# Kernel optimization log

Hardware: AMD Instinct MI355X
Metric: run time of the kernel (lower is better)

The kernel has to match this reference:

```python
import jax, jax.numpy as jnp
import numpy as np
import math

D = 1024
FFN = 4096
NHEADS = 8
HEAD_DIM = D // NHEADS
RL_DIM = 4
LN_EPS = 1e-5


def _layer_norm(x, gamma, beta):
    mu = jnp.mean(x, axis=-1, keepdims=True)
    var = jnp.var(x, axis=-1, keepdims=True)
    return (x - mu) * jax.lax.rsqrt(var + LN_EPS) * gamma + beta


def setup_inputs() -> dict:
    key = jax.random.key(0)
    ks = jax.random.split(key, 12)
    B, L = 2, 2048
    s = 1.0 / math.sqrt(D)
    inp = {
        "h": jax.random.normal(ks[0], (B, L, D), dtype=jnp.float32),
        "rh": jax.random.normal(ks[1], (B, L, RL_DIM), dtype=jnp.float32),
        "Wq": jax.random.normal(ks[2], (D, D), dtype=jnp.float32) * s,
        "Wk": jax.random.normal(ks[3], (D, D), dtype=jnp.float32) * s,
        "Wv": jax.random.normal(ks[4], (D, D), dtype=jnp.float32) * s,
        "Wo": jax.random.normal(ks[5], (D, D), dtype=jnp.float32) * s,
        "Wrk": jax.random.normal(ks[6], (RL_DIM, RL_DIM), dtype=jnp.float32) * 0.5,
        "Wrq": jax.random.normal(ks[7], (RL_DIM, RL_DIM), dtype=jnp.float32) * 0.5,
        "W1": jax.random.normal(ks[8], (D, FFN), dtype=jnp.float32) * s,
        "b1": jnp.zeros((FFN,), dtype=jnp.float32),
        "W2": jax.random.normal(ks[9], (FFN, D), dtype=jnp.float32) / math.sqrt(FFN),
        "b2": jnp.zeros((D,), dtype=jnp.float32),
        "g1": jnp.ones((D,), dtype=jnp.float32),
        "be1": jnp.zeros((D,), dtype=jnp.float32),
        "g2": jnp.ones((D,), dtype=jnp.float32),
        "be2": jnp.zeros((D,), dtype=jnp.float32),
    }
    return inp


def reference(h, rh, Wq, Wk, Wv, Wo, Wrk, Wrq, W1, b1, W2, b2, g1, be1, g2, be2):
    B, L, _ = h.shape
    q = h @ Wq  # [B, L, D]
    k = h @ Wk
    v = h @ Wv
    # Faithful to the torch code: .view() reshapes (NOT transposes).
    q_ = q.reshape(B, NHEADS, L, HEAD_DIM)
    k_ = k.reshape(B, NHEADS, L, HEAD_DIM)
    v_ = v.reshape(B, NHEADS, L, HEAD_DIM)
    k_t = k_.reshape(B, NHEADS, HEAD_DIM, L)  # reshape, not transpose, as in source
    score = jnp.einsum("bnld,bndm->bnlm", q_, k_t) / math.sqrt(HEAD_DIM)
    # relative-position bias (rl=True path)
    r_k = rh @ Wrk  # [B, L, rl_dim]
    r_q = rh @ Wrq
    r_q_ = r_q[:, None]  # [B, 1, L, rl_dim]
    r_k_t = r_k[:, None].reshape(B, 1, RL_DIM, L)  # reshape, as in source
    score = score + jnp.einsum("bnlr,bnrm->bnlm", r_q_, r_k_t) / 2.0
    attn = jax.nn.softmax(score, axis=-1)
    context = jnp.einsum("bnlm,bnmd->bnld", attn, v_)
    h_sa = context.reshape(B, L, D) @ Wo
    h1 = _layer_norm(h_sa + h, g1, be1)
    hf = jax.nn.relu(h1 @ W1 + b1) @ W2 + b2
    h2 = _layer_norm(h1 + hf, g2, be2)
    return h2
```

## Files before the change

### kernel.cpp

```cpp
#include <hip/hip_runtime.h>

typedef __bf16 bf16;
typedef __bf16 bf16x8 __attribute__((ext_vector_type(8)));
typedef __bf16 bf16x4 __attribute__((ext_vector_type(4)));
typedef float  f32x4  __attribute__((ext_vector_type(4)));

#define D_     1024
#define FFN_   4096
#define NH_    8
#define HD_    128
#define L_     2048
#define B_     2
#define ROWS_  4096
#define PAIRS_ 16
#define KT_    64
#define PSTR   72
#define ALPHA_  0.08838834764831845f
#define RSCALE_ 5.656854249492381f

__device__ __forceinline__ void async16(const bf16* g, bf16* l) {
    __builtin_amdgcn_global_load_lds(
        (const __attribute__((address_space(1))) unsigned int*)g,
        (__attribute__((address_space(3))) unsigned int*)l, 16, 0, 0);
}
__device__ __forceinline__ f32x4 MFMA(bf16x8 a, bf16x8 b, f32x4 c) {
    return __builtin_amdgcn_mfma_f32_16x16x32_bf16(a, b, c, 0, 0, 0);
}

__global__ void cvt_bf16_kernel(const float* __restrict__ in, bf16* __restrict__ out) {
    long i = ((long)blockIdx.x * 256 + threadIdx.x) * 4;
    float4 v = *(const float4*)(in + i);
    bf16x4 o = {(bf16)v.x, (bf16)v.y, (bf16)v.z, (bf16)v.w};
    *(bf16x4*)(out + i) = o;
}

template<typename TI>
__global__ void transpose_to_bf16(const TI* __restrict__ in, bf16* __restrict__ out,
                                  int r, int c, long sIn, long sOut) {
    __shared__ bf16 t[32][33];
    long zi = (long)blockIdx.z * sIn;
    long zo = (long)blockIdx.z * sOut;
    int x0 = blockIdx.x * 32, y0 = blockIdx.y * 32;
    int tx = threadIdx.x & 31, ty = threadIdx.x >> 5;
#pragma unroll
    for (int i = 0; i < 4; i++)
        t[ty + i * 8][tx] = (bf16)in[zi + (long)(y0 + ty + i * 8) * c + x0 + tx];
    __syncthreads();
#pragma unroll
    for (int i = 0; i < 4; i++)
        out[zo + (long)(x0 + ty + i * 8) * r + y0 + tx] = t[tx][ty + i * 8];
}

__global__ void rqk_kernel(const float* __restrict__ rh, const float* __restrict__ Wrq,
                           const float* __restrict__ Wrk, float* __restrict__ rq,
                           float* __restrict__ rk) {
    int t = blockIdx.x * 256 + threadIdx.x;
    float4 r = *(const float4*)(rh + (long)t * 4);
    float q[4], k[4];
#pragma unroll
    for (int c = 0; c < 4; c++) {
        q[c] = r.x * Wrq[c] + r.y * Wrq[4 + c] + r.z * Wrq[8 + c] + r.w * Wrq[12 + c];
        k[c] = r.x * Wrk[c] + r.y * Wrk[4 + c] + r.z * Wrk[8 + c] + r.w * Wrk[12 + c];
    }
    float4 qo = {q[0], q[1], q[2], q[3]};
    float4 ko = {k[0], k[1], k[2], k[3]};
    *(float4*)(rq + (long)t * 4) = qo;
    *(float4*)(rk + (long)t * 4) = ko;
}

template<int BM, int EPI>
__launch_bounds__(256)
__global__ void gemm128(const bf16* __restrict__ A, const bf16* __restrict__ Bt,
                        void* __restrict__ Cv, const float* __restrict__ bias,
                        int M, int N, int K, int lda, int ldb,
                        long sA, long sB, long sC, float alpha) {
    constexpr int RF = (BM == 128) ? 4 : 2;
    __shared__ __align__(16) bf16 As[BM * 32];
    __shared__ __align__(16) bf16 Bs[128 * 32];
    const int tid  = threadIdx.x;
    const int wave = tid >> 6, lane = tid & 63;
    const int quad = lane >> 4, mr = lane & 15;
    const int bM = blockIdx.x * BM, bN = blockIdx.y * 128;
    A  += (long)blockIdx.z * sA;
    Bt += (long)blockIdx.z * sB;
    const int wr = (wave >> 1) * (BM / 2), wc = (wave & 1) * 64;

    f32x4 acc[RF][4];
#pragma unroll
    for (int r = 0; r < RF; r++)
#pragma unroll
        for (int c = 0; c < 4; c++) { f32x4 z = {0.f, 0.f, 0.f, 0.f}; acc[r][c] = z; }

    const int scol = (lane & 3) * 8;
    const bf16* Ag0; const bf16* Ag1 = nullptr;
    if (BM == 128) {
        const int srow = wave * 32 + (lane >> 2);
        Ag0 = A + (long)(bM + srow) * lda + scol;
        Ag1 = Ag0 + (long)16 * lda;
    } else {
        const int srow = wave * 16 + (lane >> 2);
        Ag0 = A + (long)(bM + srow) * lda + scol;
    }
    const int srowB = wave * 32 + (lane >> 2);
    const bf16* Bg0 = Bt + (long)(bN + srowB) * ldb + scol;
    const bf16* Bg1 = Bg0 + (long)16 * ldb;
    bf16* AsW = As + wave * (BM == 128 ? 1024 : 512);
    bf16* BsW = Bs + wave * 1024;

    for (int k0 = 0; k0 < K; k0 += 32) {
        if (BM == 128) { async16(Ag0, AsW); async16(Ag1, AsW + 512); Ag0 += 32; Ag1 += 32; }
        else           { async16(Ag0, AsW); Ag0 += 32; }
        async16(Bg0, BsW); async16(Bg1, BsW + 512);
        Bg0 += 32; Bg1 += 32;
        __syncthreads();
        bf16x8 af[RF], bfv[4];
#pragma unroll
        for (int r = 0; r < RF; r++)
            af[r] = *(const bf16x8*)(&As[(wr + r * 16 + mr) * 32 + quad * 8]);
#pragma unroll
        for (int c = 0; c < 4; c++)
            bfv[c] = *(const bf16x8*)(&Bs[(wc + c * 16 + mr) * 32 + quad * 8]);
#pragma unroll
        for (int r = 0; r < RF; r++)
#pragma unroll
            for (int c = 0; c < 4; c++)
                acc[r][c] = MFMA(af[r], bfv[c], acc[r][c]);
        __syncthreads();
    }

    const long zC = (long)blockIdx.z * sC;
    float bias_c[4];
    if (EPI & 1) {
#pragma unroll
        for (int c = 0; c < 4; c++) bias_c[c] = bias[bN + wc + c * 16 + mr];
    }
#pragma unroll
    for (int r = 0; r < RF; r++) {
#pragma unroll
        for (int c = 0; c < 4; c++) {
            const long col = bN + wc + c * 16 + mr;
#pragma unroll
            for (int i = 0; i < 4; i++) {
                const long row = bM + wr + r * 16 + quad * 4 + i;
                float v = acc[r][c][i] * alpha;
                if (EPI & 1) v += bias_c[c];
                if (EPI & 2) v = fmaxf(v, 0.f);
                if (EPI & 4) ((bf16*)Cv)[zC + row * (long)N + col] = (bf16)v;
                else         ((float*)Cv)[zC + row * (long)N + col] = v;
            }
        }
    }
}

template<int EPI>
__launch_bounds__(512, 2)
__global__ void gemm256(const bf16* __restrict__ A, const bf16* __restrict__ Bt,
                        void* __restrict__ Cv, const float* __restrict__ bias,
                        int M, int N, int K, int lda, int ldb,
                        long sA, long sB, long sC, float alpha) {
    __shared__ __align__(16) bf16 LA[4][256 * 32];
    __shared__ __align__(16) bf16 LB[4][256 * 32];
    const int tid = threadIdx.x, wave = tid >> 6, lane = tid & 63;
    const int quad = lane >> 4, mr = lane & 15;
    const int wr = wave >> 2, wc = wave & 3;
    const int bM = blockIdx.x * 256, bN = blockIdx.y * 256;
    (void)M;
    A  += (long)blockIdx.z * sA;
    Bt += (long)blockIdx.z * sB;

    const int srow = tid >> 2;
    const int sg   = (((tid & 3) ^ ((tid >> 3) & 3))) * 8;
    const bf16* Ag = A  + (long)(bM + srow) * lda + sg;
    const bf16* Bg = Bt + (long)(bN + srow) * ldb + sg;

    auto stageA = [&](int slot, int kt) {
        const bf16* s = Ag + kt * 32;
        async16(s,                   &LA[slot][wave * 512]);
        async16(s + (long)128 * lda, &LA[slot][4096 + wave * 512]);
    };
    auto stageB = [&](int slot, int kt) {
        const bf16* s = Bg + kt * 32;
        async16(s,                   &LB[slot][wave * 512]);
        async16(s + (long)128 * ldb, &LB[slot][4096 + wave * 512]);
    };

    f32x4 acc[8][4];
#pragma unroll
    for (int f = 0; f < 8; f++)
#pragma unroll
        for (int n = 0; n < 4; n++) { f32x4 z = {0.f, 0.f, 0.f, 0.f}; acc[f][n] = z; }

    const int gsw = (quad ^ ((mr >> 1) & 3)) * 8;

    stageA(0, 0); stageB(0, 0);
    stageA(1, 1); stageB(1, 1);
    stageA(2, 2); stageB(2, 2);
    asm volatile("s_waitcnt vmcnt(8)" ::: "memory");
    __builtin_amdgcn_s_barrier();

    const int NT = K >> 5;
    for (int t = 0; t < NT; ++t) {
        const int slot = t & 3;
        const bf16* As = &LA[slot][0];
        const bf16* Bs = &LB[slot][0];

        bf16x8 a0[4], bb[4];
#pragma unroll
        for (int f = 0; f < 4; f++)
            a0[f] = *(const bf16x8*)(As + (wr * 128 + f * 16 + mr) * 32 + gsw);
#pragma unroll
        for (int n = 0; n < 4; n++)
            bb[n] = *(const bf16x8*)(Bs + (wc * 64 + n * 16 + mr) * 32 + gsw);
        if (t + 3 < NT) stageA((t + 3) & 3, t + 3);
        __builtin_amdgcn_s_barrier();
        asm volatile("s_waitcnt lgkmcnt(0)" ::: "memory");
        __builtin_amdgcn_sched_barrier(0);
        __builtin_amdgcn_s_setprio(1);
#pragma unroll
        for (int f = 0; f < 4; f++)
#pragma unroll
            for (int n = 0; n < 4; n++)
                acc[f][n] = MFMA(a0[f], bb[n], acc[f][n]);
        __builtin_amdgcn_s_setprio(0);
        __builtin_amdgcn_s_barrier();

        bf16x8 a1[4];
#pragma unroll
        for (int f = 0; f < 4; f++)
            a1[f] = *(const bf16x8*)(As + (wr * 128 + 64 + f * 16 + mr) * 32 + gsw);
        if (t + 3 < NT) stageB((t + 3) & 3, t + 3);
        __builtin_amdgcn_s_barrier();
        asm volatile("s_waitcnt lgkmcnt(0)" ::: "memory");
        __builtin_amdgcn_sched_barrier(0);
        __builtin_amdgcn_s_setprio(1);
#pragma unroll
        for (int f = 0; f < 4; f++)
#pragma unroll
            for (int n = 0; n < 4; n++)
                acc[4 + f][n] = MFMA(a1[f], bb[n], acc[4 + f][n]);
        __builtin_amdgcn_s_setprio(0);
        if (t < NT - 3)       asm volatile("s_waitcnt vmcnt(8)" ::: "memory");
        else if (t == NT - 3) asm volatile("s_waitcnt vmcnt(4)" ::: "memory");
        else if (t == NT - 2) asm volatile("s_waitcnt vmcnt(0)" ::: "memory");
        __builtin_amdgcn_s_barrier();
    }

    const long zC = (long)blockIdx.z * sC;
    float bias_c[4];
    if (EPI & 1) {
#pragma unroll
        for (int n = 0; n < 4; n++) bias_c[n] = bias[bN + wc * 64 + n * 16 + mr];
    }
#pragma unroll
    for (int f = 0; f < 8; f++) {
#pragma unroll
        for (int n = 0; n < 4; n++) {
            const long col = bN + wc * 64 + n * 16 + mr;
#pragma unroll
            for (int i = 0; i < 4; i++) {
                const long row = bM + wr * 128 + f * 16 + quad * 4 + i;
                float v = acc[f][n][i] * alpha;
                if (EPI & 1) v += bias_c[n];
                if (EPI & 2) v = fmaxf(v, 0.f);
                if (EPI & 4) ((bf16*)Cv)[zC + row * (long)N + col] = (bf16)v;
                else         ((float*)Cv)[zC + row * (long)N + col] = v;
            }
        }
    }
}

template<int SPLIT>
__launch_bounds__(256, 1)
__global__ void flash_attn(const bf16* __restrict__ qb, const bf16* __restrict__ kT,
                           const bf16* __restrict__ vT, const float* __restrict__ rq,
                           const float* __restrict__ rk, bf16* __restrict__ ctx,
                           float* __restrict__ opart, float* __restrict__ osum) {
    __shared__ __align__(16) bf16  Ksh[KT_ * HD_];
    __shared__ __align__(16) bf16  Vsh[HD_ * KT_];
    __shared__ __align__(16) float rks[4 * KT_];
    __shared__ __align__(16) bf16  Ps[4][32 * PSTR];

    const int tid = threadIdx.x, wave = tid >> 6, lane = tid & 63;
    const int quad = lane >> 4, mr = lane & 15;
    const int nwg = 256 * SPLIT;
    const int lid = blockIdx.x + (blockIdx.y << 4) + (blockIdx.z << 8);
    const int wid = (lid & 7) * (nwg >> 3) + (lid >> 3);
    const int ksp = wid >> 8;
    const int pair = (wid >> 4) & 15, b = pair >> 3;
    const int bQ = (wid & 15) * 128;
    const long PB = (long)pair * L_ * HD_;
    const bf16* Qg = qb + PB;
    const bf16* Kg = kT + PB;
    const bf16* Vg = vT + PB;
    const float* rkb = rk + (long)b * L_ * 4;

    bf16x8 Qf[2][4], Qe[2];
#pragma unroll
    for (int f = 0; f < 2; f++) {
#pragma unroll
        for (int t = 0; t < 4; t++)
            Qf[f][t] = *(const bf16x8*)(Qg + (long)(bQ + wave * 32 + f * 16 + mr) * HD_ + t * 32 + quad * 8);
        bf16x8 z = {};
        if (quad == 0) {
            float4 v = *(const float4*)(rq + ((long)b * L_ + bQ + wave * 32 + f * 16 + mr) * 4);
            z[0] = (bf16)(v.x * RSCALE_); z[1] = (bf16)(v.y * RSCALE_);
            z[2] = (bf16)(v.z * RSCALE_); z[3] = (bf16)(v.w * RSCALE_);
        }
        Qe[f] = z;
    }

    bf16x8 ones;
#pragma unroll
    for (int j = 0; j < 8; j++) ones[j] = (bf16)1.0f;

    f32x4 O[2][8], Os[2];
#pragma unroll
    for (int f = 0; f < 2; f++) {
#pragma unroll
        for (int c = 0; c < 8; c++) { f32x4 z = {0.f, 0.f, 0.f, 0.f}; O[f][c] = z; }
        f32x4 z = {0.f, 0.f, 0.f, 0.f}; Os[f] = z;
    }

    const int tile0 = ksp * ((L_ / KT_) / SPLIT);
    const int tile1 = tile0 + (L_ / KT_) / SPLIT;
    for (int kt = tile0; kt < tile1; kt++) {
        const int kt0 = kt * KT_;
#pragma unroll
        for (int it = 0; it < 4; it++) {
            int G = it * 256 + tid;
            int r1 = G >> 4, g1 = (G & 15) ^ (r1 & 15);
            async16(Kg + (long)(kt0 + r1) * HD_ + g1 * 8, &Ksh[(it * 256 + wave * 64) * 8]);
            int r2 = G >> 3, g2 = (G & 7) ^ (r2 & 7);
            async16(Vg + (long)r2 * L_ + kt0 + g2 * 8, &Vsh[(it * 256 + wave * 64) * 8]);
        }
        if (tid < 64) {
            int r3 = tid >> 4, g3 = tid & 15;
            async16((const bf16*)(rkb + (long)r3 * L_ + kt0 + g3 * 4), (bf16*)&rks[0]);
        }
        __syncthreads();

        bf16* PsW = Ps[wave];

        f32x4 sc[4][2];
        __builtin_amdgcn_s_setprio(1);
#pragma unroll
        for (int c = 0; c < 4; c++) {
            f32x4 s0 = {0.f, 0.f, 0.f, 0.f}, s1 = s0;
#pragma unroll
            for (int t = 0; t < 4; t++) {
                bf16x8 kf = *(const bf16x8*)(Ksh + (c * 16 + mr) * HD_ + (((t * 4 + quad) ^ mr) * 8));
                s0 = MFMA(Qf[0][t], kf, s0);
                s1 = MFMA(Qf[1][t], kf, s1);
            }
            bf16x8 ke = {};
            if (quad == 0) {
                ke[0] = (bf16)rks[0 * KT_ + c * 16 + mr];
                ke[1] = (bf16)rks[1 * KT_ + c * 16 + mr];
                ke[2] = (bf16)rks[2 * KT_ + c * 16 + mr];
                ke[3] = (bf16)rks[3 * KT_ + c * 16 + mr];
            }
            s0 = MFMA(Qe[0], ke, s0);
            s1 = MFMA(Qe[1], ke, s1);
            sc[c][0] = s0; sc[c][1] = s1;
        }
        __builtin_amdgcn_s_setprio(0);

#pragma unroll
        for (int f = 0; f < 2; f++) {
#pragma unroll
            for (int i = 0; i < 4; i++) {
                const int prow = (f * 16 + quad * 4 + i) * PSTR;
                PsW[prow + 0 * 16 + mr] = (bf16)__expf(sc[0][f][i] * ALPHA_);
                PsW[prow + 1 * 16 + mr] = (bf16)__expf(sc[1][f][i] * ALPHA_);
                PsW[prow + 2 * 16 + mr] = (bf16)__expf(sc[2][f][i] * ALPHA_);
                PsW[prow + 3 * 16 + mr] = (bf16)__expf(sc[3][f][i] * ALPHA_);
            }
        }

        __builtin_amdgcn_s_setprio(1);
#pragma unroll
        for (int t = 0; t < 2; t++) {
            bf16x8 pf0 = *(const bf16x8*)(PsW + (0 * 16 + mr) * PSTR + t * 32 + quad * 8);
            bf16x8 pf1 = *(const bf16x8*)(PsW + (1 * 16 + mr) * PSTR + t * 32 + quad * 8);
            Os[0] = MFMA(pf0, ones, Os[0]);
            Os[1] = MFMA(pf1, ones, Os[1]);
#pragma unroll
            for (int c2 = 0; c2 < 8; c2++) {
                bf16x8 vf = *(const bf16x8*)(Vsh + (c2 * 16 + mr) * KT_ + (((t * 4 + quad) ^ (mr & 7)) * 8));
                O[0][c2] = MFMA(pf0, vf, O[0][c2]);
                O[1][c2] = MFMA(pf1, vf, O[1][c2]);
            }
        }
        __builtin_amdgcn_s_setprio(0);
        __syncthreads();
    }

    if (SPLIT == 1) {
        bf16* Cg = ctx + PB;
#pragma unroll
        for (int f = 0; f < 2; f++)
#pragma unroll
            for (int i = 0; i < 4; i++) {
                const float inv = 1.f / Os[f][i];
                const long row = bQ + wave * 32 + f * 16 + quad * 4 + i;
#pragma unroll
                for (int c2 = 0; c2 < 8; c2++)
                    Cg[row * HD_ + c2 * 16 + mr] = (bf16)(O[f][c2][i] * inv);
            }
    } else {
        float* Og = opart + (long)ksp * ((long)PAIRS_ * L_ * HD_) + PB;
        float* Sg = osum + (long)ksp * (PAIRS_ * L_) + pair * L_;
#pragma unroll
        for (int f = 0; f < 2; f++)
#pragma unroll
            for (int i = 0; i < 4; i++) {
                const long row = bQ + wave * 32 + f * 16 + quad * 4 + i;
#pragma unroll
                for (int c2 = 0; c2 < 8; c2++)
                    Og[row * HD_ + c2 * 16 + mr] = O[f][c2][i];
                if (mr == 0) Sg[row] = Os[f][i];
            }
    }
}

template<int KS>
__global__ void flash_reduce(const float* __restrict__ op, const float* __restrict__ os,
                             bf16* __restrict__ ctx) {
    const long PLHD = (long)PAIRS_ * L_ * HD_;
    long e = ((long)blockIdx.x * 256 + threadIdx.x) * 4;
    long row = e >> 7;
    float4 a = *(const float4*)(op + e);
    float s = os[row];
#pragma unroll
    for (int z = 1; z < KS; z++) {
        float4 p = *(const float4*)(op + (long)z * PLHD + e);
        a.x += p.x; a.y += p.y; a.z += p.z; a.w += p.w;
        s += os[(long)z * PAIRS_ * L_ + row];
    }
    float inv = 1.f / s;
    bf16x4 o = {(bf16)(a.x * inv), (bf16)(a.y * inv),
                (bf16)(a.z * inv), (bf16)(a.w * inv)};
    *(bf16x4*)(ctx + e) = o;
}

__global__ void layernorm_res(const float* __restrict__ x1, const float* __restrict__ x2,
                              const float* __restrict__ g, const float* __restrict__ be,
                              float* __restrict__ outf, bf16* __restrict__ outb) {
    const int row = blockIdx.x, tid = threadIdx.x;
    const long base = (long)row * D_ + tid * 4;
    float4 a = *(const float4*)(x1 + base);
    float4 b = *(const float4*)(x2 + base);
    float x[4] = {a.x + b.x, a.y + b.y, a.z + b.z, a.w + b.w};
    float s = x[0] + x[1] + x[2] + x[3];
    float s2 = x[0] * x[0] + x[1] * x[1] + x[2] * x[2] + x[3] * x[3];
#pragma unroll
    for (int off = 32; off; off >>= 1) { s += __shfl_xor(s, off, 64); s2 += __shfl_xor(s2, off, 64); }
    __shared__ float ps[4], ps2[4];
    int wave = tid >> 6, lane = tid & 63;
    if (lane == 0) { ps[wave] = s; ps2[wave] = s2; }
    __syncthreads();
    s  = ps[0] + ps[1] + ps[2] + ps[3];
    s2 = ps2[0] + ps2[1] + ps2[2] + ps2[3];
    float mean = s * (1.f / D_);
    float var  = s2 * (1.f / D_) - mean * mean;
    float rstd = rsqrtf(var + 1e-5f);
    float4 gg = *(const float4*)(g + tid * 4);
    float4 bb = *(const float4*)(be + tid * 4);
    float y0 = (x[0] - mean) * rstd * gg.x + bb.x;
    float y1 = (x[1] - mean) * rstd * gg.y + bb.y;
    float y2 = (x[2] - mean) * rstd * gg.z + bb.z;
    float y3 = (x[3] - mean) * rstd * gg.w + bb.w;
    float4 yo = {y0, y1, y2, y3};
    *(float4*)(outf + base) = yo;
    bf16x4 ob = {(bf16)y0, (bf16)y1, (bf16)y2, (bf16)y3};
    *(bf16x4*)(outb + base) = ob;
}

template<int SK>
__global__ void layernorm_res2(const float* __restrict__ parts, const float* __restrict__ b2,
                               const float* __restrict__ x2, const float* __restrict__ g,
                               const float* __restrict__ be, float* __restrict__ outf) {
    const int row = blockIdx.x, tid = threadIdx.x;
    const long base = (long)row * D_ + tid * 4;
    float4 a = *(const float4*)(parts + base);
#pragma unroll
    for (int z = 1; z < SK; z++) {
        float4 p = *(const float4*)(parts + (long)z * ROWS_ * D_ + base);
        a.x += p.x; a.y += p.y; a.z += p.z; a.w += p.w;
    }
    float4 bb2 = *(const float4*)(b2 + tid * 4);
    float4 b = *(const float4*)(x2 + base);
    float x[4] = {a.x + bb2.x + b.x, a.y + bb2.y + b.y, a.z + bb2.z + b.z, a.w + bb2.w + b.w};
    float s = x[0] + x[1] + x[2] + x[3];
    float s2 = x[0] * x[0] + x[1] * x[1] + x[2] * x[2] + x[3] * x[3];
#pragma unroll
    for (int off = 32; off; off >>= 1) { s += __shfl_xor(s, off, 64); s2 += __shfl_xor(s2, off, 64); }
    __shared__ float ps[4], ps2[4];
    int wave = tid >> 6, lane = tid & 63;
    if (lane == 0) { ps[wave] = s; ps2[wave] = s2; }
    __syncthreads();
    s  = ps[0] + ps[1] + ps[2] + ps[3];
    s2 = ps2[0] + ps2[1] + ps2[2] + ps2[3];
    float mean = s * (1.f / D_);
    float var  = s2 * (1.f / D_) - mean * mean;
    float rstd = rsqrtf(var + 1e-5f);
    float4 gg = *(const float4*)(g + tid * 4);
    float4 bb = *(const float4*)(be + tid * 4);
    float4 yo = {(x[0] - mean) * rstd * gg.x + bb.x, (x[1] - mean) * rstd * gg.y + bb.y,
                 (x[2] - mean) * rstd * gg.z + bb.z, (x[3] - mean) * rstd * gg.w + bb.w};
    *(float4*)(outf + base) = yo;
}

extern "C" void kernel_launch(void* const* d_in, const int* in_sizes, int n_in,
                              void* d_out, int out_size, void* d_ws, size_t ws_size,
                              hipStream_t stream) {
    (void)in_sizes; (void)n_in; (void)out_size;
    const float* h   = (const float*)d_in[0];
    const float* rh  = (const float*)d_in[1];
    const float* Wq  = (const float*)d_in[2];
    const float* Wk  = (const float*)d_in[3];
    const float* Wv  = (const float*)d_in[4];
    const float* Wo  = (const float*)d_in[5];
    const float* Wrk = (const float*)d_in[6];
    const float* Wrq = (const float*)d_in[7];
    const float* W1  = (const float*)d_in[8];
    const float* b1  = (const float*)d_in[9];
    const float* W2  = (const float*)d_in[10];
    const float* b2  = (const float*)d_in[11];
    const float* g1  = (const float*)d_in[12];
    const float* be1 = (const float*)d_in[13];
    const float* g2  = (const float*)d_in[14];
    const float* be2 = (const float*)d_in[15];

    char* w = (char*)d_ws;
    size_t used = 0;
    auto alloc = [&](size_t bytes) { char* p = w + used; used += (bytes + 255) & ~(size_t)255; return p; };
    bf16*  hb   = (bf16*)alloc((size_t)ROWS_ * D_ * 2);
    bf16*  Wqt  = (bf16*)alloc((size_t)D_ * D_ * 2);
    bf16*  Wkt  = (bf16*)alloc((size_t)D_ * D_ * 2);
    bf16*  Wvt  = (bf16*)alloc((size_t)D_ * D_ * 2);
    bf16*  Wot  = (bf16*)alloc((size_t)D_ * D_ * 2);
    bf16*  W1t  = (bf16*)alloc((size_t)D_ * FFN_ * 2);
    bf16*  W2t  = (bf16*)alloc((size_t)FFN_ * D_ * 2);
    bf16*  qb   = (bf16*)alloc((size_t)ROWS_ * D_ * 2);
    bf16*  kb   = (bf16*)alloc((size_t)ROWS_ * D_ * 2);
    bf16*  vb   = (bf16*)alloc((size_t)ROWS_ * D_ * 2);
    bf16*  kT   = (bf16*)alloc((size_t)ROWS_ * D_ * 2);
    bf16*  vT   = (bf16*)alloc((size_t)ROWS_ * D_ * 2);
    float* rq   = (float*)alloc((size_t)ROWS_ * 4 * 4);
    float* rk   = (float*)alloc((size_t)ROWS_ * 4 * 4);
    float* h1   = (float*)alloc((size_t)ROWS_ * D_ * 4);

    const size_t psz    = (size_t)ROWS_ * D_ * 4;
    const size_t PLHD   = (size_t)PAIRS_ * L_ * HD_;
    const size_t needKS = 2 * PLHD * 4 + 2 * (size_t)PAIRS_ * L_ * 4;
    const size_t avail  = (ws_size > used) ? ws_size - used : 0;
    const int SK = (avail >= 4 * psz) ? 4 : (avail >= 2 * psz) ? 2 : 1;
    size_t region = (size_t)SK * psz;
    const int KS = (avail >= (needKS > region ? needKS : region)) ? 2 : 1;
    if (KS == 2 && needKS > region) region = needKS;
    float* P = (float*)alloc(region);
    float* hsa   = P;
    float* Opart = P;
    float* Osum  = P + 2 * PLHD;
    bf16* ctx = hb;
    bf16* mid = qb;
    bf16* h1b = hb;

    const dim3 blk(256);
    const dim3 blk512(512);
    const long BH = (long)L_ * HD_;

    cvt_bf16_kernel<<<ROWS_ * D_ / 1024, blk, 0, stream>>>(h, hb);
    transpose_to_bf16<float><<<dim3(32, 32, 1), blk, 0, stream>>>(Wq, Wqt, D_, D_, 0, 0);
    transpose_to_bf16<float><<<dim3(32, 32, 1), blk, 0, stream>>>(Wk, Wkt, D_, D_, 0, 0);
    transpose_to_bf16<float><<<dim3(32, 32, 1), blk, 0, stream>>>(Wv, Wvt, D_, D_, 0, 0);
    transpose_to_bf16<float><<<dim3(32, 32, 1), blk, 0, stream>>>(Wo, Wot, D_, D_, 0, 0);
    transpose_to_bf16<float><<<dim3(128, 32, 1), blk, 0, stream>>>(W1, W1t, D_, FFN_, 0, 0);
    transpose_to_bf16<float><<<dim3(32, 128, 1), blk, 0, stream>>>(W2, W2t, FFN_, D_, 0, 0);
    rqk_kernel<<<ROWS_ / 256, blk, 0, stream>>>(rh, Wrq, Wrk, rq, rk);
    gemm256<4><<<dim3(16, 4, 3), blk512, 0, stream>>>(hb, Wqt, qb, nullptr,
        ROWS_, D_, D_, D_, D_, 0, (long)D_ * D_, (long)ROWS_ * D_, 1.f);
    transpose_to_bf16<bf16><<<dim3(64, 4, PAIRS_), blk, 0, stream>>>(kb, kT, HD_, L_, BH, BH);
    transpose_to_bf16<bf16><<<dim3(4, 64, PAIRS_), blk, 0, stream>>>(vb, vT, L_, HD_, BH, BH);
    if (KS == 2) {
        flash_attn<2><<<dim3(16, 16, 2), blk, 0, stream>>>(qb, kT, vT, rq, rk, ctx, Opart, Osum);
        flash_reduce<2><<<PAIRS_ * L_ * HD_ / 1024, blk, 0, stream>>>(Opart, Osum, ctx);
    } else {
        flash_attn<1><<<dim3(16, 16, 1), blk, 0, stream>>>(qb, kT, vT, rq, rk, ctx, Opart, Osum);
    }
    gemm128<64, 0><<<dim3(64, 8, 1), blk, 0, stream>>>(ctx, Wot, hsa, nullptr,
        ROWS_, D_, D_, D_, D_, 0, 0, 0, 1.f);
    layernorm_res<<<ROWS_, blk, 0, stream>>>(hsa, h, g1, be1, h1, h1b);
    gemm256<7><<<dim3(16, 16, 1), blk512, 0, stream>>>(h1b, W1t, mid, b1,
        ROWS_, FFN_, D_, D_, D_, 0, 0, 0, 1.f);
    {
        const int KC = FFN_ / SK;
        if (SK == 4) {
            gemm256<0><<<dim3(16, 4, 4), blk512, 0, stream>>>(mid, W2t, P, nullptr,
                ROWS_, D_, KC, FFN_, FFN_, KC, KC, (long)ROWS_ * D_, 1.f);
            layernorm_res2<4><<<ROWS_, blk, 0, stream>>>(P, b2, h1, g2, be2, (float*)d_out);
        } else if (SK == 2) {
            gemm256<0><<<dim3(16, 4, 2), blk512, 0, stream>>>(mid, W2t, P, nullptr,
                ROWS_, D_, KC, FFN_, FFN_, KC, KC, (long)ROWS_ * D_, 1.f);
            layernorm_res2<2><<<ROWS_, blk, 0, stream>>>(P, b2, h1, g2, be2, (float*)d_out);
        } else {
            gemm128<128, 0><<<dim3(32, 8, 1), blk, 0, stream>>>(mid, W2t, P, nullptr,
                ROWS_, D_, FFN_, FFN_, FFN_, 0, 0, 0, 1.f);
            layernorm_res2<1><<<ROWS_, blk, 0, stream>>>(P, b2, h1, g2, be2, (float*)d_out);
        }
    }
}
```

Measured before the change: 382.6 us.

## Double-buffer flash attention K/V tiles with smaller key tile, retile Wo GEMM

The flash attention kernel now uses a 32-key tile with two LDS buffers, so the async load of the next K, V and rk tile is issued before computing on the current one, and a single waitcnt plus barrier replaces the per-tile syncthreads. The aim is to hide global-to-LDS load latency behind MFMA and exp work. The cost is twice as many loop iterations with less MFMA work per barrier. Separately, the output-projection GEMM switches from the 64-row to the 128-row gemm128 tiling with half the blocks.

```diff
diff --git a/kernel.cpp b/kernel.cpp
--- a/kernel.cpp
+++ b/kernel.cpp
@@ -13,8 +13,8 @@
 #define B_     2
 #define ROWS_  4096
 #define PAIRS_ 16
-#define KT_    64
-#define PSTR   72
+#define KT_    32
+#define PSTR   40
 #define ALPHA_  0.08838834764831845f
 #define RSCALE_ 5.656854249492381f
 
@@ -275,9 +275,9 @@
                            const bf16* __restrict__ vT, const float* __restrict__ rq,
                            const float* __restrict__ rk, bf16* __restrict__ ctx,
                            float* __restrict__ opart, float* __restrict__ osum) {
-    __shared__ __align__(16) bf16  Ksh[KT_ * HD_];
-    __shared__ __align__(16) bf16  Vsh[HD_ * KT_];
-    __shared__ __align__(16) float rks[4 * KT_];
+    __shared__ __align__(16) bf16  Ksh[2][KT_ * HD_];
+    __shared__ __align__(16) bf16  Vsh[2][HD_ * KT_];
+    __shared__ __align__(16) float rks[2][4 * KT_];
     __shared__ __align__(16) bf16  Ps[4][32 * PSTR];
 
     const int tid = threadIdx.x, wave = tid >> 6, lane = tid & 63;
@@ -294,6 +294,21 @@
     const bf16* Vg = vT + PB;
     const float* rkb = rk + (long)b * L_ * 4;
 
+    auto stage = [&](int bn, int kn0) {
+#pragma unroll
+        for (int it = 0; it < 2; it++) {
+            int G = it * 256 + tid;
+            int r1 = G >> 4, g1 = (G & 15) ^ (r1 & 15);
+            async16(Kg + (long)(kn0 + r1) * HD_ + g1 * 8, &Ksh[bn][(it * 256 + wave * 64) * 8]);
+            int r2 = G >> 2, g2 = (G & 3) ^ (r2 & 3);
+            async16(Vg + (long)r2 * L_ + kn0 + g2 * 8, &Vsh[bn][(it * 256 + wave * 64) * 8]);
+        }
+        if (tid < 32) {
+            int r3 = tid >> 3, g3 = tid & 7;
+            async16((const bf16*)(rkb + (long)r3 * L_ + kn0 + g3 * 4), (bf16*)&rks[bn][0]);
+        }
+    };
+
     bf16x8 Qf[2][4], Qe[2];
 #pragma unroll
     for (int f = 0; f < 2; f++) {
@@ -323,41 +338,38 @@
 
     const int tile0 = ksp * ((L_ / KT_) / SPLIT);
     const int tile1 = tile0 + (L_ / KT_) / SPLIT;
+
+    stage(tile0 & 1, tile0 * KT_);
+    asm volatile("s_waitcnt vmcnt(0)" ::: "memory");
+    __builtin_amdgcn_s_barrier();
+
     for (int kt = tile0; kt < tile1; kt++) {
-        const int kt0 = kt * KT_;
-#pragma unroll
-        for (int it = 0; it < 4; it++) {
-            int G = it * 256 + tid;
-            int r1 = G >> 4, g1 = (G & 15) ^ (r1 & 15);
-            async16(Kg + (long)(kt0 + r1) * HD_ + g1 * 8, &Ksh[(it * 256 + wave * 64) * 8]);
-            int r2 = G >> 3, g2 = (G & 7) ^ (r2 & 7);
-            async16(Vg + (long)r2 * L_ + kt0 + g2 * 8, &Vsh[(it * 256 + wave * 64) * 8]);
-        }
-        if (tid < 64) {
-            int r3 = tid >> 4, g3 = tid & 15;
-            async16((const bf16*)(rkb + (long)r3 * L_ + kt0 + g3 * 4), (bf16*)&rks[0]);
-        }
-        __syncthreads();
+        const int cur = kt & 1;
+        const bool hn = (kt + 1 < tile1);
+        if (hn) stage(cur ^ 1, (kt + 1) * KT_);
 
         bf16* PsW = Ps[wave];
-
-        f32x4 sc[4][2];
+        const bf16*  Kcur = Ksh[cur];
+        const bf16*  Vcur = Vsh[cur];
+        const float* rkc  = rks[cur];
+
+        f32x4 sc[2][2];
         __builtin_amdgcn_s_setprio(1);
 #pragma unroll
-        for (int c = 0; c < 4; c++) {
+        for (int c = 0; c < 2; c++) {
             f32x4 s0 = {0.f, 0.f, 0.f, 0.f}, s1 = s0;
 #pragma unroll
             for (int t = 0; t < 4; t++) {
-                bf16x8 kf = *(const bf16x8*)(Ksh + (c * 16 + mr) * HD_ + (((t * 4 + quad) ^ mr) * 8));
+                bf16x8 kf = *(const bf16x8*)(Kcur + (c * 16 + mr) * HD_ + (((t * 4 + quad) ^ mr) * 8));
                 s0 = MFMA(Qf[0][t], kf, s0);
                 s1 = MFMA(Qf[1][t], kf, s1);
             }
             bf16x8 ke = {};
             if (quad == 0) {
-                ke[0] = (bf16)rks[0 * KT_ + c * 16 + mr];
-                ke[1] = (bf16)rks[1 * KT_ + c * 16 + mr];
-                ke[2] = (bf16)rks[2 * KT_ + c * 16 + mr];
-                ke[3] = (bf16)rks[3 * KT_ + c * 16 + mr];
+                ke[0] = (bf16)rkc[0 * KT_ + c * 16 + mr];
+                ke[1] = (bf16)rkc[1 * KT_ + c * 16 + mr];
+                ke[2] = (bf16)rkc[2 * KT_ + c * 16 + mr];
+                ke[3] = (bf16)rkc[3 * KT_ + c * 16 + mr];
             }
             s0 = MFMA(Qe[0], ke, s0);
             s1 = MFMA(Qe[1], ke, s1);
@@ -372,27 +384,28 @@
                 const int prow = (f * 16 + quad * 4 + i) * PSTR;
                 PsW[prow + 0 * 16 + mr] = (bf16)__expf(sc[0][f][i] * ALPHA_);
                 PsW[prow + 1 * 16 + mr] = (bf16)__expf(sc[1][f][i] * ALPHA_);
-                PsW[prow + 2 * 16 + mr] = (bf16)__expf(sc[2][f][i] * ALPHA_);
-                PsW[prow + 3 * 16 + mr] = (bf16)__expf(sc[3][f][i] * ALPHA_);
             }
         }
 
         __builtin_amdgcn_s_setprio(1);
-#pragma unroll
-        for (int t = 0; t < 2; t++) {
-            bf16x8 pf0 = *(const bf16x8*)(PsW + (0 * 16 + mr) * PSTR + t * 32 + quad * 8);
-            bf16x8 pf1 = *(const bf16x8*)(PsW + (1 * 16 + mr) * PSTR + t * 32 + quad * 8);
+        {
+            bf16x8 pf0 = *(const bf16x8*)(PsW + (0 * 16 + mr) * PSTR + quad * 8);
+            bf16x8 pf1 = *(const bf16x8*)(PsW + (1 * 16 + mr) * PSTR + quad * 8);
             Os[0] = MFMA(pf0, ones, Os[0]);
             Os[1] = MFMA(pf1, ones, Os[1]);
 #pragma unroll
             for (int c2 = 0; c2 < 8; c2++) {
-                bf16x8 vf = *(const bf16x8*)(Vsh + (c2 * 16 + mr) * KT_ + (((t * 4 + quad) ^ (mr & 7)) * 8));
+                bf16x8 vf = *(const bf16x8*)(Vcur + (c2 * 16 + mr) * KT_ + ((quad ^ (mr & 3)) * 8));
                 O[0][c2] = MFMA(pf0, vf, O[0][c2]);
                 O[1][c2] = MFMA(pf1, vf, O[1][c2]);
             }
         }
         __builtin_amdgcn_s_setprio(0);
-        __syncthreads();
+
+        if (hn) {
+            asm volatile("s_waitcnt vmcnt(0)" ::: "memory");
+            __builtin_amdgcn_s_barrier();
+        }
     }
 
     if (SPLIT == 1) {
@@ -589,7 +602,7 @@
     } else {
         flash_attn<1><<<dim3(16, 16, 1), blk, 0, stream>>>(qb, kT, vT, rq, rk, ctx, Opart, Osum);
     }
-    gemm128<64, 0><<<dim3(64, 8, 1), blk, 0, stream>>>(ctx, Wot, hsa, nullptr,
+    gemm128<128, 0><<<dim3(32, 8, 1), blk, 0, stream>>>(ctx, Wot, hsa, nullptr,
         ROWS_, D_, D_, D_, D_, 0, 0, 0, 1.f);
     layernorm_res<<<ROWS_, blk, 0, stream>>>(hsa, h, g1, be1, h1, h1b);
     gemm256<7><<<dim3(16, 16, 1), blk512, 0, stream>>>(h1b, W1t, mid, b1,
```

New measurement: 395.0 us. +3.2%, slower.

## Replace 256x256 GEMM with 128x256 tile, 4-wave, double-buffered kernel

Applied to the files above, without the earlier changes.

Swaps the 512-thread 256x256 GEMM, which used a 4-stage async LDS pipeline and split A halves, for a 256-thread kernel computing 128x256 tiles. Each wave owns a 64-column slice across all 128 rows, and the kernel uses simple two-slot double buffering with one barrier per k-step. Grids double in the x dimension, and the Wo projection GEMM moves to a 128-wide tile variant. This trades pipeline depth and per-block reuse for more blocks and lower sync overhead, at the risk of exposing global-load latency with only one stage of prefetch.

```diff
diff --git a/kernel.cpp b/kernel.cpp
--- a/kernel.cpp
+++ b/kernel.cpp
@@ -153,17 +153,16 @@
 }
 
 template<int EPI>
-__launch_bounds__(512, 2)
-__global__ void gemm256(const bf16* __restrict__ A, const bf16* __restrict__ Bt,
-                        void* __restrict__ Cv, const float* __restrict__ bias,
-                        int M, int N, int K, int lda, int ldb,
-                        long sA, long sB, long sC, float alpha) {
-    __shared__ __align__(16) bf16 LA[4][256 * 32];
-    __shared__ __align__(16) bf16 LB[4][256 * 32];
+__launch_bounds__(256)
+__global__ void gemmA(const bf16* __restrict__ A, const bf16* __restrict__ Bt,
+                      void* __restrict__ Cv, const float* __restrict__ bias,
+                      int M, int N, int K, int lda, int ldb,
+                      long sA, long sB, long sC, float alpha) {
+    __shared__ __align__(16) bf16 As[2][128 * 32];
+    __shared__ __align__(16) bf16 Bs[2][256 * 32];
     const int tid = threadIdx.x, wave = tid >> 6, lane = tid & 63;
     const int quad = lane >> 4, mr = lane & 15;
-    const int wr = wave >> 2, wc = wave & 3;
-    const int bM = blockIdx.x * 256, bN = blockIdx.y * 256;
+    const int bM = blockIdx.x * 128, bN = blockIdx.y * 256;
     (void)M;
     A  += (long)blockIdx.z * sA;
     Bt += (long)blockIdx.z * sB;
@@ -173,16 +172,16 @@
     const bf16* Ag = A  + (long)(bM + srow) * lda + sg;
     const bf16* Bg = Bt + (long)(bN + srow) * ldb + sg;
 
-    auto stageA = [&](int slot, int kt) {
-        const bf16* s = Ag + kt * 32;
-        async16(s,                   &LA[slot][wave * 512]);
-        async16(s + (long)128 * lda, &LA[slot][4096 + wave * 512]);
+    auto stage = [&](int slot, int t) {
+        const bf16* a = Ag + t * 32;
+        async16(a,                   &As[slot][wave * 512]);
+        async16(a + (long)64 * lda,  &As[slot][2048 + wave * 512]);
+        const bf16* bs = Bg + t * 32;
+        async16(bs,                  &Bs[slot][wave * 512]);
+        async16(bs + (long)64 * ldb, &Bs[slot][2048 + wave * 512]);
+        async16(bs + (long)128 * ldb, &Bs[slot][4096 + wave * 512]);
+        async16(bs + (long)192 * ldb, &Bs[slot][6144 + wave * 512]);
     };
-    auto stageB = [&](int slot, int kt) {
-        const bf16* s = Bg + kt * 32;
-        async16(s,                   &LB[slot][wave * 512]);
-        async16(s + (long)128 * ldb, &LB[slot][4096 + wave * 512]);
-    };
 
     f32x4 acc[8][4];
 #pragma unroll
@@ -192,56 +191,32 @@
 
     const int gsw = (quad ^ ((mr >> 1) & 3)) * 8;
 
-    stageA(0, 0); stageB(0, 0);
-    stageA(1, 1); stageB(1, 1);
-    stageA(2, 2); stageB(2, 2);
-    asm volatile("s_waitcnt vmcnt(8)" ::: "memory");
+    const int NT = K >> 5;
+    stage(0, 0);
+    asm volatile("s_waitcnt vmcnt(0)" ::: "memory");
     __builtin_amdgcn_s_barrier();
 
-    const int NT = K >> 5;
     for (int t = 0; t < NT; ++t) {
-        const int slot = t & 3;
-        const bf16* As = &LA[slot][0];
-        const bf16* Bs = &LB[slot][0];
-
-        bf16x8 a0[4], bb[4];
-#pragma unroll
-        for (int f = 0; f < 4; f++)
-            a0[f] = *(const bf16x8*)(As + (wr * 128 + f * 16 + mr) * 32 + gsw);
+        const int slot = t & 1;
+        if (t + 1 < NT) stage(slot ^ 1, t + 1);
+
+        bf16x8 af[8], bfv[4];
+#pragma unroll
+        for (int f = 0; f < 8; f++)
+            af[f] = *(const bf16x8*)(&As[slot][(f * 16 + mr) * 32 + gsw]);
 #pragma unroll
         for (int n = 0; n < 4; n++)
-            bb[n] = *(const bf16x8*)(Bs + (wc * 64 + n * 16 + mr) * 32 + gsw);
-        if (t + 3 < NT) stageA((t + 3) & 3, t + 3);
-        __builtin_amdgcn_s_barrier();
+            bfv[n] = *(const bf16x8*)(&Bs[slot][(wave * 64 + n * 16 + mr) * 32 + gsw]);
         asm volatile("s_waitcnt lgkmcnt(0)" ::: "memory");
         __builtin_amdgcn_sched_barrier(0);
         __builtin_amdgcn_s_setprio(1);
 #pragma unroll
-        for (int f = 0; f < 4; f++)
+        for (int f = 0; f < 8; f++)
 #pragma unroll
             for (int n = 0; n < 4; n++)
-                acc[f][n] = MFMA(a0[f], bb[n], acc[f][n]);
+                acc[f][n] = MFMA(af[f], bfv[n], acc[f][n]);
         __builtin_amdgcn_s_setprio(0);
-        __builtin_amdgcn_s_barrier();
-
-        bf16x8 a1[4];
-#pragma unroll
-        for (int f = 0; f < 4; f++)
-            a1[f] = *(const bf16x8*)(As + (wr * 128 + 64 + f * 16 + mr) * 32 + gsw);
-        if (t + 3 < NT) stageB((t + 3) & 3, t + 3);
-        __builtin_amdgcn_s_barrier();
-        asm volatile("s_waitcnt lgkmcnt(0)" ::: "memory");
-        __builtin_amdgcn_sched_barrier(0);
-        __builtin_amdgcn_s_setprio(1);
-#pragma unroll
-        for (int f = 0; f < 4; f++)
-#pragma unroll
-            for (int n = 0; n < 4; n++)
-                acc[4 + f][n] = MFMA(a1[f], bb[n], acc[4 + f][n]);
-        __builtin_amdgcn_s_setprio(0);
-        if (t < NT - 3)       asm volatile("s_waitcnt vmcnt(8)" ::: "memory");
-        else if (t == NT - 3) asm volatile("s_waitcnt vmcnt(4)" ::: "memory");
-        else if (t == NT - 2) asm volatile("s_waitcnt vmcnt(0)" ::: "memory");
+        if (t + 1 < NT) asm volatile("s_waitcnt vmcnt(0)" ::: "memory");
         __builtin_amdgcn_s_barrier();
     }
 
@@ -249,16 +224,16 @@
     float bias_c[4];
     if (EPI & 1) {
 #pragma unroll
-        for (int n = 0; n < 4; n++) bias_c[n] = bias[bN + wc * 64 + n * 16 + mr];
+        for (int n = 0; n < 4; n++) bias_c[n] = bias[bN + wave * 64 + n * 16 + mr];
     }
 #pragma unroll
     for (int f = 0; f < 8; f++) {
 #pragma unroll
         for (int n = 0; n < 4; n++) {
-            const long col = bN + wc * 64 + n * 16 + mr;
+            const long col = bN + wave * 64 + n * 16 + mr;
 #pragma unroll
             for (int i = 0; i < 4; i++) {
-                const long row = bM + wr * 128 + f * 16 + quad * 4 + i;
+                const long row = bM + f * 16 + quad * 4 + i;
                 float v = acc[f][n][i] * alpha;
                 if (EPI & 1) v += bias_c[n];
                 if (EPI & 2) v = fmaxf(v, 0.f);
@@ -568,7 +543,6 @@
     bf16* h1b = hb;
 
     const dim3 blk(256);
-    const dim3 blk512(512);
     const long BH = (long)L_ * HD_;
 
     cvt_bf16_kernel<<<ROWS_ * D_ / 1024, blk, 0, stream>>>(h, hb);
@@ -579,7 +553,7 @@
     transpose_to_bf16<float><<<dim3(128, 32, 1), blk, 0, stream>>>(W1, W1t, D_, FFN_, 0, 0);
     transpose_to_bf16<float><<<dim3(32, 128, 1), blk, 0, stream>>>(W2, W2t, FFN_, D_, 0, 0);
     rqk_kernel<<<ROWS_ / 256, blk, 0, stream>>>(rh, Wrq, Wrk, rq, rk);
-    gemm256<4><<<dim3(16, 4, 3), blk512, 0, stream>>>(hb, Wqt, qb, nullptr,
+    gemmA<4><<<dim3(32, 4, 3), blk, 0, stream>>>(hb, Wqt, qb, nullptr,
         ROWS_, D_, D_, D_, D_, 0, (long)D_ * D_, (long)ROWS_ * D_, 1.f);
     transpose_to_bf16<bf16><<<dim3(64, 4, PAIRS_), blk, 0, stream>>>(kb, kT, HD_, L_, BH, BH);
     transpose_to_bf16<bf16><<<dim3(4, 64, PAIRS_), blk, 0, stream>>>(vb, vT, L_, HD_, BH, BH);
@@ -589,19 +563,19 @@
     } else {
         flash_attn<1><<<dim3(16, 16, 1), blk, 0, stream>>>(qb, kT, vT, rq, rk, ctx, Opart, Osum);
     }
-    gemm128<64, 0><<<dim3(64, 8, 1), blk, 0, stream>>>(ctx, Wot, hsa, nullptr,
+    gemm128<128, 0><<<dim3(32, 8, 1), blk, 0, stream>>>(ctx, Wot, hsa, nullptr,
         ROWS_, D_, D_, D_, D_, 0, 0, 0, 1.f);
     layernorm_res<<<ROWS_, blk, 0, stream>>>(hsa, h, g1, be1, h1, h1b);
-    gemm256<7><<<dim3(16, 16, 1), blk512, 0, stream>>>(h1b, W1t, mid, b1,
+    gemmA<7><<<dim3(32, 16, 1), blk, 0, stream>>>(h1b, W1t, mid, b1,
         ROWS_, FFN_, D_, D_, D_, 0, 0, 0, 1.f);
     {
         const int KC = FFN_ / SK;
         if (SK == 4) {
-            gemm256<0><<<dim3(16, 4, 4), blk512, 0, stream>>>(mid, W2t, P, nullptr,
+            gemmA<0><<<dim3(32, 4, 4), blk, 0, stream>>>(mid, W2t, P, nullptr,
                 ROWS_, D_, KC, FFN_, FFN_, KC, KC, (long)ROWS_ * D_, 1.f);
             layernorm_res2<4><<<ROWS_, blk, 0, stream>>>(P, b2, h1, g2, be2, (float*)d_out);
         } else if (SK == 2) {
-            gemm256<0><<<dim3(16, 4, 2), blk512, 0, stream>>>(mid, W2t, P, nullptr,
+            gemmA<0><<<dim3(32, 4, 2), blk, 0, stream>>>(mid, W2t, P, nullptr,
                 ROWS_, D_, KC, FFN_, FFN_, KC, KC, (long)ROWS_ * D_, 1.f);
             layernorm_res2<2><<<ROWS_, blk, 0, stream>>>(P, b2, h1, g2, be2, (float*)d_out);
         } else {
```

Result: slower. 476.5 us (+24.5%).
